# Optimization experiments

Measured on AMD Instinct MI355X. Metric: run time of the kernel, lower is better.

The kernel has to match this reference:

```python
import jax, jax.numpy as jnp
import numpy as np

B, T, C, H = 2, 2048, 1024, 16
D = C // H  # head_dim = 64


def wheel_softmax(scores):
    """Wheel-arithmetic softmax: total division, bot (0/0) positions -> 0.
    Rows that are entirely -inf yield sum==0 -> bot -> filled with 0.0,
    matching wheel_out.to_numpy_safe(bot_fill=0.0, inf_fill=0.0)."""
    m = jnp.max(scores, axis=-1, keepdims=True)
    safe_m = jnp.where(jnp.isfinite(m), m, 0.0)
    e = jnp.exp(scores - safe_m)          # -inf entries -> 0
    z = jnp.sum(e, axis=-1, keepdims=True)
    ok = z > 0
    return jnp.where(ok, e / jnp.where(ok, z, 1.0), 0.0)


def setup_inputs() -> dict:
    key = jax.random.key(0)
    ks = jax.random.split(key, 12)
    s = 1.0 / np.sqrt(C)
    inp = {
        "query": jax.random.normal(ks[0], (B, T, C), jnp.float32),
        "key": jax.random.normal(ks[1], (B, T, C), jnp.float32),
        "value": jax.random.normal(ks[2], (B, T, C), jnp.float32),
        "q_w": jax.random.normal(ks[3], (C, C), jnp.float32) * s,
        "q_b": jax.random.normal(ks[4], (C,), jnp.float32) * 0.01,
        "k_w": jax.random.normal(ks[5], (C, C), jnp.float32) * s,
        "k_b": jax.random.normal(ks[6], (C,), jnp.float32) * 0.01,
        "v_w": jax.random.normal(ks[7], (C, C), jnp.float32) * s,
        "v_b": jax.random.normal(ks[8], (C,), jnp.float32) * 0.01,
        "o_w": jax.random.normal(ks[9], (C, C), jnp.float32) * s,
        "o_b": jax.random.normal(ks[10], (C,), jnp.float32) * 0.01,
        "key_padding_mask": jax.random.randint(ks[11], (B, T), 0, 2).astype(bool),
    }
    return inp


def reference(query, key, value, q_w, q_b, k_w, k_b, v_w, v_b, o_w, o_b, key_padding_mask):
    scale = D ** -0.5
    def proj(x, w, b):
        # nn.Linear: x @ w.T + b ; reshape to [B,H,T,D]
        y = jnp.einsum("btc,oc->bto", x, w) + b
        return y.reshape(B, T, H, D).transpose(0, 2, 1, 3)
    Q = proj(query, q_w, q_b)
    K = proj(key, k_w, k_b)
    V = proj(value, v_w, v_b)
    scores = jnp.einsum("bhqd,bhkd->bhqk", Q, K) * scale
    scores = jnp.where(key_padding_mask[:, None, None, :], -jnp.inf, scores)
    weights = wheel_softmax(scores)  # dropout=0 -> identity
    out = jnp.einsum("bhqk,bhkd->bhqd", weights, V)
    out = out.transpose(0, 2, 1, 3).reshape(B, T, C)
    out = jnp.einsum("btc,oc->bto", out, o_w) + o_b
    return (out, weights)
```

## Files before the change

kernel.cpp:

```cpp
#include <hip/hip_runtime.h>
#include <math.h>


typedef _Float16 f16;
typedef _Float16 f16x2 __attribute__((ext_vector_type(2)));
typedef _Float16 f16x4 __attribute__((ext_vector_type(4)));
typedef _Float16 f16x8 __attribute__((ext_vector_type(8)));
typedef float  f32x2  __attribute__((ext_vector_type(2)));
typedef float  f32x4  __attribute__((ext_vector_type(4)));

#define MFMAH(a, b, c)  __builtin_amdgcn_mfma_f32_16x16x32_f16((a), (b), (c), 0, 0, 0)

__device__ __forceinline__ void gload16(void* lds, const void* g) {
  __builtin_amdgcn_global_load_lds((__attribute__((address_space(1))) void*)(g),
                                   (__attribute__((address_space(3))) void*)(lds),
                                   16, 0, 0);
}

__global__ __launch_bounds__(256) void conv_f16(const float* __restrict__ q, const float* __restrict__ k,
                                                const float* __restrict__ v, const float* __restrict__ qw,
                                                const float* __restrict__ kw, const float* __restrict__ vw,
                                                const float* __restrict__ ow, f16* __restrict__ xf) {
  long long i = ((long long)blockIdx.x * 256 + threadIdx.x) * 4;
  const float* src;
  long long off;
  if (i < 4194304)       { src = q;  off = 0; }
  else if (i < 8388608)  { src = k;  off = 4194304; }
  else if (i < 12582912) { src = v;  off = 8388608; }
  else if (i < 13631488) { src = qw; off = 12582912; }
  else if (i < 14680064) { src = kw; off = 13631488; }
  else if (i < 15728640) { src = vw; off = 14680064; }
  else                   { src = ow; off = 15728640; }
  f32x4 val = *(const f32x4*)(src + (i - off));
  f16x4 h;
#pragma unroll
  for (int r = 0; r < 4; ++r) h[r] = (f16)val[r];
  *(f16x4*)(xf + i) = h;
}

__device__ __forceinline__ void stage_tile(f16* lds, const f16* g, int row0, int kc, int tid) {
#pragma unroll
  for (int j = 0; j < 2; ++j) {
    int chunk = j * 256 + tid;
    int r = chunk >> 2, cpos = chunk & 3;
    int csrc = cpos ^ ((r >> 1) & 3);
    gload16((char*)lds + chunk * 16,
            (const char*)(g + (size_t)(row0 + r) * 1024 + kc) + csrc * 16);
  }
}

__device__ __forceinline__ f16x8 frag_ld(const f16* lds, int row, int g) {
  int pos = g ^ ((row >> 1) & 3);
  return *(const f16x8*)((const char*)lds + row * 64 + pos * 16);
}

__device__ __forceinline__ void gemm_core(const f16* A, const f16* X, int o0, int t0, int tid,
                                          f16* sA, f16* sB, f32x4 acc[4][4]) {
  int wid = tid >> 6, lane = tid & 63;
  int wm = wid >> 1, wn = wid & 1, g = lane >> 4, r15 = lane & 15;
  for (int kc = 0; kc < 1024; kc += 32) {
    __syncthreads();
    stage_tile(sA, A, o0, kc, tid);
    stage_tile(sB, X, t0, kc, tid);
    __syncthreads();
    f16x8 a[4], x[4];
#pragma unroll
    for (int f = 0; f < 4; ++f) {
      a[f] = frag_ld(sA, wm * 64 + f * 16 + r15, g);
      x[f] = frag_ld(sB, wn * 64 + f * 16 + r15, g);
    }
#pragma unroll
    for (int fm = 0; fm < 4; ++fm)
#pragma unroll
      for (int fn = 0; fn < 4; ++fn)
        acc[fm][fn] = MFMAH(a[fm], x[fn], acc[fm][fn]);
  }
}

__global__ __launch_bounds__(256) void gemm_qkv(const f16* __restrict__ xf,
                                                const float* __restrict__ q_b, const float* __restrict__ k_b,
                                                const float* __restrict__ v_b,
                                                f16* __restrict__ Qf, f16* __restrict__ Kf,
                                                f16* __restrict__ VT2) {
  __shared__ f16 sA[4096], sB[4096];
  int z = blockIdx.z;
  int tid = threadIdx.x;
  int wid = tid >> 6, lane = tid & 63;
  int wm = wid >> 1, wn = wid & 1, g = lane >> 4, r15 = lane & 15;
  f32x4 acc[4][4] = {};
  if (z == 2) {
    const f16* X = xf + 8388608;
    const f16* W = xf + 14680064;
    int o0 = blockIdx.x * 128, t0 = blockIdx.y * 128;
    gemm_core(X, W, t0, o0, tid, sA, sB, acc);
#pragma unroll
    for (int fm = 0; fm < 4; ++fm)
#pragma unroll
      for (int fn = 0; fn < 4; ++fn) {
        int tb = t0 + wm * 64 + fm * 16 + 4 * g;
        int o  = o0 + wn * 64 + fn * 16 + r15;
        int bb = tb >> 11, tl = tb & 2047, hh = o >> 6, dd = o & 63;
        int ch = tl >> 5, c = tl & 31;
        int slotbase = (c < 16) ? ((c >> 2) << 3) : ((((c - 16) >> 2) << 3) + 4);
        float bo = v_b[o];
        f16x4 v4;
#pragma unroll
        for (int r = 0; r < 4; ++r) v4[r] = (f16)(acc[fm][fn][r] + bo);
        *(f16x4*)(VT2 + ((((size_t)bb * 16 + hh) * 64 + ch) * 64 + dd) * 32 + slotbase) = v4;
      }
  } else {
    const f16* A = xf + (z ? 13631488 : 12582912);
    const f16* X = xf + (z ? 4194304 : 0);
    const float* bias = z ? k_b : q_b;
    f16* Yf = z ? Kf : Qf;
    float scale = z ? 1.0f : 0.125f;
    int o0 = blockIdx.x * 128, t0 = blockIdx.y * 128;
    gemm_core(A, X, o0, t0, tid, sA, sB, acc);
#pragma unroll
    for (int fm = 0; fm < 4; ++fm)
#pragma unroll
      for (int fn = 0; fn < 4; ++fn) {
        int ob = o0 + wm * 64 + fm * 16 + 4 * g;
        int t  = t0 + wn * 64 + fn * 16 + r15;
        int bb = t >> 11, tl = t & 2047, hh = ob >> 6, dd = ob & 63;
        size_t base = (((size_t)bb * 16 + hh) * 2048 + tl) * 64 + dd;
        f16x4 vh;
#pragma unroll
        for (int r = 0; r < 4; ++r)
          vh[r] = (f16)((acc[fm][fn][r] + bias[ob + r]) * scale);
        *(f16x4*)(Yf + base) = vh;
      }
  }
}

__global__ __launch_bounds__(256) void gemm_o(const f16* __restrict__ xf, const f16* __restrict__ Abuf,
                                              const float* __restrict__ o_b, float* __restrict__ OutF) {
  __shared__ f16 sA[4096], sB[4096];
  const f16* A = xf + 15728640;
  int tid = threadIdx.x;
  int o0 = blockIdx.x * 128, t0 = blockIdx.y * 128;
  int wid = tid >> 6, lane = tid & 63;
  int wm = wid >> 1, wn = wid & 1, g = lane >> 4, r15 = lane & 15;
  f32x4 acc[4][4] = {};
  gemm_core(A, Abuf, o0, t0, tid, sA, sB, acc);
#pragma unroll
  for (int fm = 0; fm < 4; ++fm)
#pragma unroll
    for (int fn = 0; fn < 4; ++fn) {
      int ob = o0 + wm * 64 + fm * 16 + 4 * g;
      int t  = t0 + wn * 64 + fn * 16 + r15;
      f32x4 v;
#pragma unroll
      for (int r = 0; r < 4; ++r) v[r] = acc[fm][fn][r] + o_b[ob + r];
      *(f32x4*)(OutF + (size_t)t * 1024 + ob) = v;
    }
}

__global__ __launch_bounds__(512, 4) void attn_kernel(
    const f16* __restrict__ Qf, const f16* __restrict__ Kf,
    const f16* __restrict__ VT2, const int* __restrict__ mask,
    float* __restrict__ wout, f16* __restrict__ Abuf) {
  __shared__ f16 kstage[8][2][1024];
  __shared__ f16 pvh[8][16][72];
  __shared__ float ps[128];
  __shared__ float rz[16];
  int tid = threadIdx.x;
  int wid = tid >> 6, lane = tid & 63;
  int g = lane >> 4, r15 = lane & 15;
  int qt = blockIdx.x & 127, bh = blockIdx.x >> 7;
  int b = bh >> 4, h = bh & 15;
  int q0 = qt * 16;

  if (blockIdx.x & 1) __builtin_amdgcn_s_sleep(24);

  const f16* qp = Qf + ((size_t)bh * 2048 + q0 + r15) * 64 + 8 * g;
  f16x8 qh0 = *(const f16x8*)(qp);
  f16x8 qh1 = *(const f16x8*)(qp + 32);

  const int* mp = mask + b * 2048 + wid * 256 + 4 * g;
  unsigned long long mb = 0;
#pragma unroll
  for (int t = 0; t < 16; ++t) {
    int4 ma = *(const int4*)(mp + t * 16);
    mb |= ((ma.x ? 1ull : 0ull) << (4 * t)) | ((ma.y ? 1ull : 0ull) << (4 * t + 1)) |
          ((ma.z ? 1ull : 0ull) << (4 * t + 2)) | ((ma.w ? 1ull : 0ull) << (4 * t + 3));
  }

  f16* kb0 = &kstage[wid][0][0];
  f16* kb1 = &kstage[wid][1][0];
  const f16* ksrcA = Kf + ((size_t)bh * 2048 + wid * 256 + (lane >> 3)) * 64 +
                     (((lane & 7) ^ ((lane >> 3) & 7)) * 8);
  const f16* ksrcB = ksrcA + 8 * 64;

  gload16(kb0, ksrcA);
  gload16(kb0 + 512, ksrcB);
  gload16(kb1, ksrcA + 1024);
  gload16(kb1 + 512, ksrcB + 1024);
  asm volatile("s_waitcnt vmcnt(2)" ::: "memory");
  int key = r15 & 7;
  f16x8 c0 = *(const f16x8*)(kb0 + r15 * 64 + ((g ^ key) * 8));
  f16x8 c1 = *(const f16x8*)(kb0 + r15 * 64 + (((g + 4) ^ key) * 8));

  float psum = 0.f;
  f16x4 p16[16];
#pragma unroll
  for (int s = 0; s < 16; ++s) {
    if (s < 14) {
      asm volatile("s_waitcnt lgkmcnt(0)" ::: "memory");
      f16* nb = (s & 1) ? kb1 : kb0;
      gload16(nb, ksrcA + (s + 2) * 1024);
      gload16(nb + 512, ksrcB + (s + 2) * 1024);
    }
    f16x8 n0, n1;
    if (s < 15) {
      if (s < 14) asm volatile("s_waitcnt vmcnt(2)" ::: "memory");
      else        asm volatile("s_waitcnt vmcnt(0)" ::: "memory");
      const f16* nt = ((s + 1) & 1) ? kb1 : kb0;
      n0 = *(const f16x8*)(nt + r15 * 64 + ((g ^ key) * 8));
      n1 = *(const f16x8*)(nt + r15 * 64 + (((g + 4) ^ key) * 8));
    }
    f32x4 sc = {0.f, 0.f, 0.f, 0.f};
    sc = MFMAH(c0, qh0, sc);
    sc = MFMAH(c1, qh1, sc);
    f16x4 pk;
#pragma unroll
    for (int r = 0; r < 4; ++r) {
      float e = ((mb >> (4 * s + r)) & 1) ? 0.f : __expf(sc[r]);
      psum += e;
      pk[r] = (f16)e;
    }
    p16[s] = pk;
    c0 = n0;
    c1 = n1;
  }

  psum += __shfl_xor(psum, 16);
  psum += __shfl_xor(psum, 32);
  if (lane < 16) ps[lane * 8 + wid] = psum;
  __syncthreads();

  if (tid < 128) {
    float z = ps[tid];
#pragma unroll
    for (int m = 1; m <= 4; m <<= 1) z += __shfl_xor(z, m);
    if ((tid & 7) == 0) rz[tid >> 3] = (z > 0.f) ? 1.0f / z : 0.0f;
  }
  __syncthreads();

  f32x4 acc[4] = {};
  {
    float rzv = rz[r15];
    float* wb = wout + ((size_t)bh * 2048 + q0 + r15) * 2048 + wid * 256 + 4 * g;
    const f16* vb = VT2 + (((size_t)bh * 64 + wid * 8) * 64 + r15) * 32 + g * 8;
    f16x8 v0 = *(const f16x8*)(vb);
    f16x8 v1 = *(const f16x8*)(vb + 512);
    f16x8 v2 = *(const f16x8*)(vb + 1024);
    f16x8 v3 = *(const f16x8*)(vb + 1536);
#pragma unroll
    for (int t = 0; t < 8; ++t) {
      f16x8 n0, n1, n2, n3;
      if (t < 7) {
        const f16* nvb = vb + (t + 1) * 2048;
        n0 = *(const f16x8*)(nvb);
        n1 = *(const f16x8*)(nvb + 512);
        n2 = *(const f16x8*)(nvb + 1024);
        n3 = *(const f16x8*)(nvb + 1536);
      }
#pragma unroll
      for (int u = 0; u < 2; ++u) {
        int s = 2 * t + u;
        f16x4 pk = p16[s];
        f32x4 wv;
#pragma unroll
        for (int r = 0; r < 4; ++r) wv[r] = (float)pk[r] * rzv;
        __builtin_nontemporal_store(wv, (f32x4*)(wb + s * 16));
      }
      f16x8 af = __builtin_shufflevector(p16[2 * t], p16[2 * t + 1], 0, 1, 2, 3, 4, 5, 6, 7);
      acc[0] = MFMAH(af, v0, acc[0]);
      acc[1] = MFMAH(af, v1, acc[1]);
      acc[2] = MFMAH(af, v2, acc[2]);
      acc[3] = MFMAH(af, v3, acc[3]);
      v0 = n0; v1 = n1; v2 = n2; v3 = n3;
    }
#pragma unroll
    for (int dt = 0; dt < 4; ++dt)
#pragma unroll
      for (int r = 0; r < 4; ++r)
        pvh[wid][4 * g + r][dt * 16 + r15] = (f16)acc[dt][r];
  }
  __syncthreads();

  {
    int q = tid >> 5, d = (tid & 31) * 2;
    float a0 = 0.f, a1 = 0.f;
#pragma unroll
    for (int w8 = 0; w8 < 8; ++w8) {
      f16x2 v = *(const f16x2*)&pvh[w8][q][d];
      a0 += (float)v[0];
      a1 += (float)v[1];
    }
    float rzq = rz[q];
    f16x2 o2 = {(f16)(a0 * rzq), (f16)(a1 * rzq)};
    *(f16x2*)(Abuf + ((size_t)b * 2048 + q0 + q) * 1024 + h * 64 + d) = o2;
  }
}

extern "C" void kernel_launch(void* const* d_in, const int* in_sizes, int n_in,
                              void* d_out, int out_size, void* d_ws, size_t ws_size,
                              hipStream_t stream) {
  const float* query = (const float*)d_in[0];
  const float* key_i = (const float*)d_in[1];
  const float* value = (const float*)d_in[2];
  const float* q_w = (const float*)d_in[3];
  const float* q_b = (const float*)d_in[4];
  const float* k_w = (const float*)d_in[5];
  const float* k_b = (const float*)d_in[6];
  const float* v_w = (const float*)d_in[7];
  const float* v_b = (const float*)d_in[8];
  const float* o_w = (const float*)d_in[9];
  const float* o_b = (const float*)d_in[10];
  const int* mask = (const int*)d_in[11];
  float* out = (float*)d_out;
  float* wout = out + 4194304;

  const size_t XFB = 16777216ull * 2;
  const size_t QB = 4194304ull * 2;
  if (ws_size < XFB + 2 * QB) return;
  f16* xf = (f16*)d_ws;
  f16* Qf = (f16*)((char*)d_ws + XFB);
  f16* Kf = (f16*)((char*)d_ws + XFB + QB);
  f16* VT2 = xf;
  f16* Abuf = xf + 4194304;
  VT2 = (f16*)((char*)d_ws + XFB + 2 * QB - 0);
  VT2  = (f16*)((char*)d_ws + XFB + 2 * QB);
  Abuf = (f16*)((char*)d_ws + XFB + 3 * QB);
  if (ws_size < XFB + 4 * QB) return;

  conv_f16<<<16384, 256, 0, stream>>>(query, key_i, value, q_w, k_w, v_w, o_w, xf);
  gemm_qkv<<<dim3(8, 32, 3), 256, 0, stream>>>(xf, q_b, k_b, v_b, Qf, Kf, VT2);
  attn_kernel<<<4096, 512, 0, stream>>>(Qf, Kf, VT2, mask, wout, Abuf);
  gemm_o<<<dim3(8, 32), 256, 0, stream>>>(xf, Abuf, o_b, out);
}
```

Measured before the change: 264.2 us.

## Stage attention weights through LDS for row-contiguous coalesced stores

The attention kernel now writes the fp16 probabilities into a per-wave LDS scratch area that reuses the K staging buffer. It reads them back transposed so each lane stores 16-byte chunks along a row, and each row of the 2048-wide fp32 weights output gets 512 contiguous bytes instead of scattered 16-byte pieces. This targets write coalescing on the dominant weights-output traffic. It also raises the launch-bounds occupancy hint from 4 to 6, removes the s_sleep stagger on odd blocks, and tidies the workspace pointer setup. The costs are extra LDS traffic, a waitcnt, and possible register pressure from the higher occupancy target.

```diff
diff --git a/kernel.cpp b/kernel.cpp
--- a/kernel.cpp
+++ b/kernel.cpp
@@ -156,11 +156,11 @@
     }
 }
 
-__global__ __launch_bounds__(512, 4) void attn_kernel(
+__global__ __launch_bounds__(512, 6) void attn_kernel(
     const f16* __restrict__ Qf, const f16* __restrict__ Kf,
     const f16* __restrict__ VT2, const int* __restrict__ mask,
     float* __restrict__ wout, f16* __restrict__ Abuf) {
-  __shared__ f16 kstage[8][2][1024];
+  __shared__ char smemA[8][4224];
   __shared__ f16 pvh[8][16][72];
   __shared__ float ps[128];
   __shared__ float rz[16];
@@ -171,8 +171,6 @@
   int b = bh >> 4, h = bh & 15;
   int q0 = qt * 16;
 
-  if (blockIdx.x & 1) __builtin_amdgcn_s_sleep(24);
-
   const f16* qp = Qf + ((size_t)bh * 2048 + q0 + r15) * 64 + 8 * g;
   f16x8 qh0 = *(const f16x8*)(qp);
   f16x8 qh1 = *(const f16x8*)(qp + 32);
@@ -186,8 +184,8 @@
           ((ma.z ? 1ull : 0ull) << (4 * t + 2)) | ((ma.w ? 1ull : 0ull) << (4 * t + 3));
   }
 
-  f16* kb0 = &kstage[wid][0][0];
-  f16* kb1 = &kstage[wid][1][0];
+  f16* kb0 = (f16*)&smemA[wid][0];
+  f16* kb1 = (f16*)&smemA[wid][2048];
   const f16* ksrcA = Kf + ((size_t)bh * 2048 + wid * 256 + (lane >> 3)) * 64 +
                      (((lane & 7) ^ ((lane >> 3) & 7)) * 8);
   const f16* ksrcB = ksrcA + 8 * 64;
@@ -249,8 +247,9 @@
 
   f32x4 acc[4] = {};
   {
-    float rzv = rz[r15];
-    float* wb = wout + ((size_t)bh * 2048 + q0 + r15) * 2048 + wid * 256 + 4 * g;
+    char* pst = &smemA[wid][0];
+    int c5 = lane & 31, hi5 = lane >> 5;
+    float* wrowbase = wout + ((size_t)bh * 2048 + q0) * 2048 + wid * 256;
     const f16* vb = VT2 + (((size_t)bh * 64 + wid * 8) * 64 + r15) * 32 + g * 8;
     f16x8 v0 = *(const f16x8*)(vb);
     f16x8 v1 = *(const f16x8*)(vb + 512);
@@ -266,14 +265,26 @@
         n2 = *(const f16x8*)(nvb + 1024);
         n3 = *(const f16x8*)(nvb + 1536);
       }
-#pragma unroll
-      for (int u = 0; u < 2; ++u) {
-        int s = 2 * t + u;
-        f16x4 pk = p16[s];
-        f32x4 wv;
-#pragma unroll
-        for (int r = 0; r < 4; ++r) wv[r] = (float)pk[r] * rzv;
-        __builtin_nontemporal_store(wv, (f32x4*)(wb + s * 16));
+      if (t == 0 || t == 4) {
+        int hb = (t >> 2) * 8;
+#pragma unroll
+        for (int s2 = 0; s2 < 8; ++s2)
+          *(f16x4*)(pst + r15 * 264 + s2 * 32 + g * 8) = p16[hb + s2];
+        asm volatile("s_waitcnt lgkmcnt(0)" ::: "memory");
+      }
+      {
+        int hh2 = t >> 2, rbase = (t & 3) * 4;
+#pragma unroll
+        for (int u = 0; u < 2; ++u) {
+          int row = rbase + 2 * u + hi5;
+          f16x4 pv4 = *(const f16x4*)(pst + row * 264 + c5 * 8);
+          float rzr = rz[row];
+          f32x4 wv;
+#pragma unroll
+          for (int r = 0; r < 4; ++r) wv[r] = (float)pv4[r] * rzr;
+          __builtin_nontemporal_store(wv,
+              (f32x4*)(wrowbase + (size_t)row * 2048 + hh2 * 128 + 4 * c5));
+        }
       }
       f16x8 af = __builtin_shufflevector(p16[2 * t], p16[2 * t + 1], 0, 1, 2, 3, 4, 5, 6, 7);
       acc[0] = MFMAH(af, v0, acc[0]);
@@ -325,16 +336,12 @@
 
   const size_t XFB = 16777216ull * 2;
   const size_t QB = 4194304ull * 2;
-  if (ws_size < XFB + 2 * QB) return;
-  f16* xf = (f16*)d_ws;
-  f16* Qf = (f16*)((char*)d_ws + XFB);
-  f16* Kf = (f16*)((char*)d_ws + XFB + QB);
-  f16* VT2 = xf;
-  f16* Abuf = xf + 4194304;
-  VT2 = (f16*)((char*)d_ws + XFB + 2 * QB - 0);
-  VT2  = (f16*)((char*)d_ws + XFB + 2 * QB);
-  Abuf = (f16*)((char*)d_ws + XFB + 3 * QB);
   if (ws_size < XFB + 4 * QB) return;
+  f16* xf   = (f16*)d_ws;
+  f16* Qf   = (f16*)((char*)d_ws + XFB);
+  f16* Kf   = (f16*)((char*)d_ws + XFB + QB);
+  f16* VT2  = (f16*)((char*)d_ws + XFB + 2 * QB);
+  f16* Abuf = (f16*)((char*)d_ws + XFB + 3 * QB);
 
   conv_f16<<<16384, 256, 0, stream>>>(query, key_i, value, q_w, k_w, v_w, o_w, xf);
   gemm_qkv<<<dim3(8, 32, 3), 256, 0, stream>>>(xf, q_b, k_b, v_b, Qf, Kf, VT2);
```

Result: faster. 258.9 us (-2.0%).

## Split attention into row-sum pass and main pass with larger query tiles

Applied to the files above, without the earlier changes.

Replaces the single attention kernel with two kernels. The first computes per-row softmax normalizers using 128-query tiles per block, so each loaded K tile is reused across eight query groups. The second recomputes scores for 32-query tiles, normalizes them on the fly, writes the weights and does P·V, which doubles K/V reuse per block and keeps fewer probabilities in registers. The cost is computing QK^T twice plus an extra launch and a small Zinv buffer, in exchange for more K reuse and less register pressure.

```diff
diff --git a/kernel.cpp b/kernel.cpp
--- a/kernel.cpp
+++ b/kernel.cpp
@@ -10,6 +10,7 @@
 typedef float  f32x4  __attribute__((ext_vector_type(4)));
 
 #define MFMAH(a, b, c)  __builtin_amdgcn_mfma_f32_16x16x32_f16((a), (b), (c), 0, 0, 0)
+#define SB0() __builtin_amdgcn_sched_barrier(0)
 
 __device__ __forceinline__ void gload16(void* lds, const void* g) {
   __builtin_amdgcn_global_load_lds((__attribute__((address_space(1))) void*)(g),
@@ -156,26 +157,17 @@
     }
 }
 
-__global__ __launch_bounds__(512, 4) void attn_kernel(
+__global__ __launch_bounds__(512, 4) void attn_rowsum(
     const f16* __restrict__ Qf, const f16* __restrict__ Kf,
-    const f16* __restrict__ VT2, const int* __restrict__ mask,
-    float* __restrict__ wout, f16* __restrict__ Abuf) {
+    const int* __restrict__ mask, float* __restrict__ Zinv) {
   __shared__ f16 kstage[8][2][1024];
-  __shared__ f16 pvh[8][16][72];
-  __shared__ float ps[128];
-  __shared__ float rz[16];
+  __shared__ float ps[128][8];
   int tid = threadIdx.x;
   int wid = tid >> 6, lane = tid & 63;
   int g = lane >> 4, r15 = lane & 15;
-  int qt = blockIdx.x & 127, bh = blockIdx.x >> 7;
-  int b = bh >> 4, h = bh & 15;
-  int q0 = qt * 16;
-
-  if (blockIdx.x & 1) __builtin_amdgcn_s_sleep(24);
-
-  const f16* qp = Qf + ((size_t)bh * 2048 + q0 + r15) * 64 + 8 * g;
-  f16x8 qh0 = *(const f16x8*)(qp);
-  f16x8 qh1 = *(const f16x8*)(qp + 32);
+  int qt = blockIdx.x, bh = blockIdx.y;
+  int b = bh >> 4;
+  int q0 = qt * 128;
 
   const int* mp = mask + b * 2048 + wid * 256 + 4 * g;
   unsigned long long mb = 0;
@@ -185,123 +177,197 @@
     mb |= ((ma.x ? 1ull : 0ull) << (4 * t)) | ((ma.y ? 1ull : 0ull) << (4 * t + 1)) |
           ((ma.z ? 1ull : 0ull) << (4 * t + 2)) | ((ma.w ? 1ull : 0ull) << (4 * t + 3));
   }
-
+  f16x8 qf[8][2];
+#pragma unroll
+  for (int qg = 0; qg < 8; ++qg) {
+    const f16* qp = Qf + ((size_t)bh * 2048 + q0 + qg * 16 + r15) * 64 + 8 * g;
+    qf[qg][0] = *(const f16x8*)(qp);
+    qf[qg][1] = *(const f16x8*)(qp + 32);
+  }
+  SB0();
   f16* kb0 = &kstage[wid][0][0];
   f16* kb1 = &kstage[wid][1][0];
   const f16* ksrcA = Kf + ((size_t)bh * 2048 + wid * 256 + (lane >> 3)) * 64 +
                      (((lane & 7) ^ ((lane >> 3) & 7)) * 8);
-  const f16* ksrcB = ksrcA + 8 * 64;
-
-  gload16(kb0, ksrcA);
-  gload16(kb0 + 512, ksrcB);
-  gload16(kb1, ksrcA + 1024);
-  gload16(kb1 + 512, ksrcB + 1024);
-  asm volatile("s_waitcnt vmcnt(2)" ::: "memory");
+  const f16* ksrcB = ksrcA + 512;
+  gload16(kb0, ksrcA); gload16(kb0 + 512, ksrcB);
+  SB0();
+  gload16(kb1, ksrcA + 1024); gload16(kb1 + 512, ksrcB + 1024);
+  SB0();
+
+  float psum[8] = {};
   int key = r15 & 7;
-  f16x8 c0 = *(const f16x8*)(kb0 + r15 * 64 + ((g ^ key) * 8));
-  f16x8 c1 = *(const f16x8*)(kb0 + r15 * 64 + (((g + 4) ^ key) * 8));
-
-  float psum = 0.f;
-  f16x4 p16[16];
 #pragma unroll
   for (int s = 0; s < 16; ++s) {
+    if (s < 15) asm volatile("s_waitcnt vmcnt(2)" ::: "memory");
+    else        asm volatile("s_waitcnt vmcnt(0)" ::: "memory");
+    const f16* kt = (s & 1) ? kb1 : kb0;
+    f16x8 c0 = *(const f16x8*)(kt + r15 * 64 + ((g ^ key) * 8));
+    f16x8 c1 = *(const f16x8*)(kt + r15 * 64 + (((g + 4) ^ key) * 8));
+    asm volatile("s_waitcnt lgkmcnt(0)" ::: "memory");
     if (s < 14) {
-      asm volatile("s_waitcnt lgkmcnt(0)" ::: "memory");
       f16* nb = (s & 1) ? kb1 : kb0;
       gload16(nb, ksrcA + (s + 2) * 1024);
       gload16(nb + 512, ksrcB + (s + 2) * 1024);
     }
-    f16x8 n0, n1;
-    if (s < 15) {
-      if (s < 14) asm volatile("s_waitcnt vmcnt(2)" ::: "memory");
-      else        asm volatile("s_waitcnt vmcnt(0)" ::: "memory");
-      const f16* nt = ((s + 1) & 1) ? kb1 : kb0;
-      n0 = *(const f16x8*)(nt + r15 * 64 + ((g ^ key) * 8));
-      n1 = *(const f16x8*)(nt + r15 * 64 + (((g + 4) ^ key) * 8));
-    }
-    f32x4 sc = {0.f, 0.f, 0.f, 0.f};
-    sc = MFMAH(c0, qh0, sc);
-    sc = MFMAH(c1, qh1, sc);
-    f16x4 pk;
+    SB0();
+#pragma unroll
+    for (int qg = 0; qg < 8; ++qg) {
+      f32x4 sc = {0.f, 0.f, 0.f, 0.f};
+      sc = MFMAH(c0, qf[qg][0], sc);
+      sc = MFMAH(c1, qf[qg][1], sc);
+#pragma unroll
+      for (int r = 0; r < 4; ++r) {
+        float e = ((mb >> (4 * s + r)) & 1) ? 0.f : __expf(sc[r]);
+        psum[qg] += e;
+      }
+    }
+  }
+#pragma unroll
+  for (int qg = 0; qg < 8; ++qg) {
+    float z = psum[qg];
+    z += __shfl_xor(z, 16);
+    z += __shfl_xor(z, 32);
+    if (lane < 16) ps[qg * 16 + lane][wid] = z;
+  }
+  __syncthreads();
+  if (tid < 128) {
+    float z = 0.f;
+#pragma unroll
+    for (int w8 = 0; w8 < 8; ++w8) z += ps[tid][w8];
+    Zinv[(size_t)bh * 2048 + q0 + tid] = (z > 0.f) ? 1.0f / z : 0.0f;
+  }
+}
+
+__global__ __launch_bounds__(512, 4) void attn_main(
+    const f16* __restrict__ Qf, const f16* __restrict__ Kf,
+    const f16* __restrict__ VT2, const int* __restrict__ mask,
+    const float* __restrict__ Zinv, float* __restrict__ wout, f16* __restrict__ Abuf) {
+  __shared__ f16 kstage[8][2][1024];
+  __shared__ f16 qlds[2048];
+  __shared__ f16 pvh[8][32][72];
+  int tid = threadIdx.x;
+  int wid = tid >> 6, lane = tid & 63;
+  int g = lane >> 4, r15 = lane & 15;
+  int qt = blockIdx.x, bh = blockIdx.y;
+  int b = bh >> 4, h = bh & 15;
+  int q0 = qt * 32;
+
+  const int* mp = mask + b * 2048 + wid * 256 + 4 * g;
+  unsigned long long mb = 0;
+#pragma unroll
+  for (int t = 0; t < 16; ++t) {
+    int4 ma = *(const int4*)(mp + t * 16);
+    mb |= ((ma.x ? 1ull : 0ull) << (4 * t)) | ((ma.y ? 1ull : 0ull) << (4 * t + 1)) |
+          ((ma.z ? 1ull : 0ull) << (4 * t + 2)) | ((ma.w ? 1ull : 0ull) << (4 * t + 3));
+  }
+  float rz0 = Zinv[(size_t)bh * 2048 + q0 + r15];
+  float rz1 = Zinv[(size_t)bh * 2048 + q0 + 16 + r15];
+  if (wid < 4) {
+    int row = wid * 8 + (lane >> 3);
+    const f16* qsrc = Qf + ((size_t)bh * 2048 + q0 + row) * 64 + (((lane & 7) ^ (row & 7)) * 8);
+    gload16(qlds + wid * 512, qsrc);
+  }
+  SB0();
+  f16* kb0 = &kstage[wid][0][0];
+  f16* kb1 = &kstage[wid][1][0];
+  const f16* ksrcA = Kf + ((size_t)bh * 2048 + wid * 256 + (lane >> 3)) * 64 +
+                     (((lane & 7) ^ ((lane >> 3) & 7)) * 8);
+  const f16* ksrcB = ksrcA + 512;
+  gload16(kb0, ksrcA); gload16(kb0 + 512, ksrcB);
+  SB0();
+  gload16(kb1, ksrcA + 1024); gload16(kb1 + 512, ksrcB + 1024);
+  SB0();
+  asm volatile("s_waitcnt vmcnt(4)" ::: "memory");
+  __builtin_amdgcn_s_barrier();
+
+  int key = r15 & 7;
+  float* wb0 = wout + ((size_t)bh * 2048 + q0 + r15) * 2048 + wid * 256 + 4 * g;
+  float* wb1 = wb0 + (size_t)16 * 2048;
+  const f16* vb = VT2 + (((size_t)bh * 64 + wid * 8) * 64 + r15) * 32 + g * 8;
+
+  f32x4 acc0[4] = {}, acc1[4] = {};
+  f16x4 pp0, pp1;
+  f16x8 v0, v1, v2, v3;
+#pragma unroll
+  for (int s = 0; s < 16; ++s) {
+    if (s == 0)       asm volatile("s_waitcnt vmcnt(2)" ::: "memory");
+    else if (s == 1)  asm volatile("s_waitcnt vmcnt(8)" ::: "memory");
+    else if (s == 15) asm volatile("s_waitcnt vmcnt(8)" ::: "memory");
+    else              asm volatile("s_waitcnt vmcnt(10)" ::: "memory");
+    const f16* kt = (s & 1) ? kb1 : kb0;
+    f16x8 c0  = *(const f16x8*)(kt + r15 * 64 + ((g ^ key) * 8));
+    f16x8 c1  = *(const f16x8*)(kt + r15 * 64 + (((g + 4) ^ key) * 8));
+    f16x8 q00 = *(const f16x8*)(qlds + r15 * 64 + ((g ^ key) * 8));
+    f16x8 q01 = *(const f16x8*)(qlds + r15 * 64 + (((g + 4) ^ key) * 8));
+    f16x8 q10 = *(const f16x8*)(qlds + (16 + r15) * 64 + ((g ^ key) * 8));
+    f16x8 q11 = *(const f16x8*)(qlds + (16 + r15) * 64 + (((g + 4) ^ key) * 8));
+    asm volatile("s_waitcnt lgkmcnt(0)" ::: "memory");
+    if (s < 14) {
+      f16* nb = (s & 1) ? kb1 : kb0;
+      gload16(nb, ksrcA + (s + 2) * 1024);
+      gload16(nb + 512, ksrcB + (s + 2) * 1024);
+    }
+    SB0();
+    if ((s & 1) == 0) {
+      const f16* vp = vb + (s >> 1) * 2048;
+      v0 = *(const f16x8*)(vp);
+      v1 = *(const f16x8*)(vp + 512);
+      v2 = *(const f16x8*)(vp + 1024);
+      v3 = *(const f16x8*)(vp + 1536);
+    }
+    f32x4 s0 = {0.f, 0.f, 0.f, 0.f}, s1 = {0.f, 0.f, 0.f, 0.f};
+    s0 = MFMAH(c0, q00, s0);
+    s0 = MFMAH(c1, q01, s0);
+    s1 = MFMAH(c0, q10, s1);
+    s1 = MFMAH(c1, q11, s1);
+    f32x4 w0v, w1v;
+    f16x4 pk0, pk1;
 #pragma unroll
     for (int r = 0; r < 4; ++r) {
-      float e = ((mb >> (4 * s + r)) & 1) ? 0.f : __expf(sc[r]);
-      psum += e;
-      pk[r] = (f16)e;
-    }
-    p16[s] = pk;
-    c0 = n0;
-    c1 = n1;
-  }
-
-  psum += __shfl_xor(psum, 16);
-  psum += __shfl_xor(psum, 32);
-  if (lane < 16) ps[lane * 8 + wid] = psum;
+      float e0 = ((mb >> (4 * s + r)) & 1) ? 0.f : __expf(s0[r]);
+      float e1 = ((mb >> (4 * s + r)) & 1) ? 0.f : __expf(s1[r]);
+      float x0 = e0 * rz0, x1 = e1 * rz1;
+      w0v[r] = x0; pk0[r] = (f16)x0;
+      w1v[r] = x1; pk1[r] = (f16)x1;
+    }
+    __builtin_nontemporal_store(w0v, (f32x4*)(wb0 + s * 16));
+    __builtin_nontemporal_store(w1v, (f32x4*)(wb1 + s * 16));
+    if (s & 1) {
+      f16x8 af0 = __builtin_shufflevector(pp0, pk0, 0, 1, 2, 3, 4, 5, 6, 7);
+      f16x8 af1 = __builtin_shufflevector(pp1, pk1, 0, 1, 2, 3, 4, 5, 6, 7);
+      acc0[0] = MFMAH(af0, v0, acc0[0]);
+      acc1[0] = MFMAH(af1, v0, acc1[0]);
+      acc0[1] = MFMAH(af0, v1, acc0[1]);
+      acc1[1] = MFMAH(af1, v1, acc1[1]);
+      acc0[2] = MFMAH(af0, v2, acc0[2]);
+      acc1[2] = MFMAH(af1, v2, acc1[2]);
+      acc0[3] = MFMAH(af0, v3, acc0[3]);
+      acc1[3] = MFMAH(af1, v3, acc1[3]);
+    }
+    pp0 = pk0;
+    pp1 = pk1;
+  }
+
+#pragma unroll
+  for (int dt = 0; dt < 4; ++dt)
+#pragma unroll
+    for (int r = 0; r < 4; ++r) {
+      pvh[wid][4 * g + r][dt * 16 + r15] = (f16)acc0[dt][r];
+      pvh[wid][16 + 4 * g + r][dt * 16 + r15] = (f16)acc1[dt][r];
+    }
   __syncthreads();
 
-  if (tid < 128) {
-    float z = ps[tid];
-#pragma unroll
-    for (int m = 1; m <= 4; m <<= 1) z += __shfl_xor(z, m);
-    if ((tid & 7) == 0) rz[tid >> 3] = (z > 0.f) ? 1.0f / z : 0.0f;
-  }
-  __syncthreads();
-
-  f32x4 acc[4] = {};
   {
-    float rzv = rz[r15];
-    float* wb = wout + ((size_t)bh * 2048 + q0 + r15) * 2048 + wid * 256 + 4 * g;
-    const f16* vb = VT2 + (((size_t)bh * 64 + wid * 8) * 64 + r15) * 32 + g * 8;
-    f16x8 v0 = *(const f16x8*)(vb);
-    f16x8 v1 = *(const f16x8*)(vb + 512);
-    f16x8 v2 = *(const f16x8*)(vb + 1024);
-    f16x8 v3 = *(const f16x8*)(vb + 1536);
-#pragma unroll
-    for (int t = 0; t < 8; ++t) {
-      f16x8 n0, n1, n2, n3;
-      if (t < 7) {
-        const f16* nvb = vb + (t + 1) * 2048;
-        n0 = *(const f16x8*)(nvb);
-        n1 = *(const f16x8*)(nvb + 512);
-        n2 = *(const f16x8*)(nvb + 1024);
-        n3 = *(const f16x8*)(nvb + 1536);
-      }
-#pragma unroll
-      for (int u = 0; u < 2; ++u) {
-        int s = 2 * t + u;
-        f16x4 pk = p16[s];
-        f32x4 wv;
-#pragma unroll
-        for (int r = 0; r < 4; ++r) wv[r] = (float)pk[r] * rzv;
-        __builtin_nontemporal_store(wv, (f32x4*)(wb + s * 16));
-      }
-      f16x8 af = __builtin_shufflevector(p16[2 * t], p16[2 * t + 1], 0, 1, 2, 3, 4, 5, 6, 7);
-      acc[0] = MFMAH(af, v0, acc[0]);
-      acc[1] = MFMAH(af, v1, acc[1]);
-      acc[2] = MFMAH(af, v2, acc[2]);
-      acc[3] = MFMAH(af, v3, acc[3]);
-      v0 = n0; v1 = n1; v2 = n2; v3 = n3;
-    }
-#pragma unroll
-    for (int dt = 0; dt < 4; ++dt)
-#pragma unroll
-      for (int r = 0; r < 4; ++r)
-        pvh[wid][4 * g + r][dt * 16 + r15] = (f16)acc[dt][r];
-  }
-  __syncthreads();
-
-  {
-    int q = tid >> 5, d = (tid & 31) * 2;
-    float a0 = 0.f, a1 = 0.f;
+    int q = tid >> 4, d4 = (tid & 15) * 4;
+    float a0 = 0.f, a1 = 0.f, a2 = 0.f, a3 = 0.f;
 #pragma unroll
     for (int w8 = 0; w8 < 8; ++w8) {
-      f16x2 v = *(const f16x2*)&pvh[w8][q][d];
-      a0 += (float)v[0];
-      a1 += (float)v[1];
-    }
-    float rzq = rz[q];
-    f16x2 o2 = {(f16)(a0 * rzq), (f16)(a1 * rzq)};
-    *(f16x2*)(Abuf + ((size_t)b * 2048 + q0 + q) * 1024 + h * 64 + d) = o2;
+      f16x4 v = *(const f16x4*)&pvh[w8][q][d4];
+      a0 += (float)v[0]; a1 += (float)v[1]; a2 += (float)v[2]; a3 += (float)v[3];
+    }
+    f16x4 o4 = {(f16)a0, (f16)a1, (f16)a2, (f16)a3};
+    *(f16x4*)(Abuf + ((size_t)b * 2048 + q0 + q) * 1024 + h * 64 + d4) = o4;
   }
 }
 
@@ -325,19 +391,18 @@
 
   const size_t XFB = 16777216ull * 2;
   const size_t QB = 4194304ull * 2;
-  if (ws_size < XFB + 2 * QB) return;
-  f16* xf = (f16*)d_ws;
-  f16* Qf = (f16*)((char*)d_ws + XFB);
-  f16* Kf = (f16*)((char*)d_ws + XFB + QB);
-  f16* VT2 = xf;
-  f16* Abuf = xf + 4194304;
-  VT2 = (f16*)((char*)d_ws + XFB + 2 * QB - 0);
-  VT2  = (f16*)((char*)d_ws + XFB + 2 * QB);
-  Abuf = (f16*)((char*)d_ws + XFB + 3 * QB);
-  if (ws_size < XFB + 4 * QB) return;
+  const size_t ZB = 65536ull * 4;
+  if (ws_size < XFB + 4 * QB + ZB) return;
+  f16* xf    = (f16*)d_ws;
+  f16* Qf    = (f16*)((char*)d_ws + XFB);
+  f16* Kf    = (f16*)((char*)d_ws + XFB + QB);
+  f16* VT2   = (f16*)((char*)d_ws + XFB + 2 * QB);
+  f16* Abuf  = (f16*)((char*)d_ws + XFB + 3 * QB);
+  float* Zinv = (float*)((char*)d_ws + XFB + 4 * QB);
 
   conv_f16<<<16384, 256, 0, stream>>>(query, key_i, value, q_w, k_w, v_w, o_w, xf);
   gemm_qkv<<<dim3(8, 32, 3), 256, 0, stream>>>(xf, q_b, k_b, v_b, Qf, Kf, VT2);
-  attn_kernel<<<4096, 512, 0, stream>>>(Qf, Kf, VT2, mask, wout, Abuf);
+  attn_rowsum<<<dim3(16, 32), 512, 0, stream>>>(Qf, Kf, mask, Zinv);
+  attn_main<<<dim3(64, 32), 512, 0, stream>>>(Qf, Kf, VT2, mask, Zinv, wout, Abuf);
   gemm_o<<<dim3(8, 32), 256, 0, stream>>>(xf, Abuf, o_b, out);
 }
```

New measurement: 528.3 us. 2x slower.

## Split attention into row-sum pre-pass and streaming weight-writing main kernel

Applied to the files above, without the earlier changes.

Adds a separate kernel that computes softmax denominators (inverse row sums) for 128 queries per block, reusing each staged K tile across 8 query groups. The main attention kernel then reads the precomputed inverse sums, so it can normalize and stream the fp32 weights out inside the QK loop. This removes the two block-wide syncs and the deferred store phase, which lets the weight writes overlap with compute, and the occupancy hint is raised. The cost is computing QK^T and exp a second time plus an extra launch.

```diff
diff --git a/kernel.cpp b/kernel.cpp
--- a/kernel.cpp
+++ b/kernel.cpp
@@ -156,14 +156,90 @@
     }
 }
 
-__global__ __launch_bounds__(512, 4) void attn_kernel(
+__global__ __launch_bounds__(512, 4) void attn_rowsum(
+    const f16* __restrict__ Qf, const f16* __restrict__ Kf,
+    const int* __restrict__ mask, float* __restrict__ Zinv) {
+  __shared__ f16 kstage[8][2][1024];
+  __shared__ float ps[128][8];
+  int tid = threadIdx.x;
+  int wid = tid >> 6, lane = tid & 63;
+  int g = lane >> 4, r15 = lane & 15;
+  int qt = blockIdx.x, bh = blockIdx.y;
+  int b = bh >> 4;
+  int q0 = qt * 128;
+
+  const int* mp = mask + b * 2048 + wid * 256 + 4 * g;
+  unsigned long long mb = 0;
+#pragma unroll
+  for (int t = 0; t < 16; ++t) {
+    int4 ma = *(const int4*)(mp + t * 16);
+    mb |= ((ma.x ? 1ull : 0ull) << (4 * t)) | ((ma.y ? 1ull : 0ull) << (4 * t + 1)) |
+          ((ma.z ? 1ull : 0ull) << (4 * t + 2)) | ((ma.w ? 1ull : 0ull) << (4 * t + 3));
+  }
+  f16x8 qf[8][2];
+#pragma unroll
+  for (int qg = 0; qg < 8; ++qg) {
+    const f16* qp = Qf + ((size_t)bh * 2048 + q0 + qg * 16 + r15) * 64 + 8 * g;
+    qf[qg][0] = *(const f16x8*)(qp);
+    qf[qg][1] = *(const f16x8*)(qp + 32);
+  }
+  f16* kb0 = &kstage[wid][0][0];
+  f16* kb1 = &kstage[wid][1][0];
+  const f16* ksrcA = Kf + ((size_t)bh * 2048 + wid * 256 + (lane >> 3)) * 64 +
+                     (((lane & 7) ^ ((lane >> 3) & 7)) * 8);
+  const f16* ksrcB = ksrcA + 512;
+  gload16(kb0, ksrcA); gload16(kb0 + 512, ksrcB);
+  gload16(kb1, ksrcA + 1024); gload16(kb1 + 512, ksrcB + 1024);
+
+  float psum[8] = {};
+  int key = r15 & 7;
+#pragma unroll
+  for (int s = 0; s < 16; ++s) {
+    if (s < 15) asm volatile("s_waitcnt vmcnt(2)" ::: "memory");
+    else        asm volatile("s_waitcnt vmcnt(0)" ::: "memory");
+    const f16* kt = (s & 1) ? kb1 : kb0;
+    f16x8 c0 = *(const f16x8*)(kt + r15 * 64 + ((g ^ key) * 8));
+    f16x8 c1 = *(const f16x8*)(kt + r15 * 64 + (((g + 4) ^ key) * 8));
+    asm volatile("s_waitcnt lgkmcnt(0)" ::: "memory");
+    if (s < 14) {
+      f16* nb = (s & 1) ? kb1 : kb0;
+      gload16(nb, ksrcA + (s + 2) * 1024);
+      gload16(nb + 512, ksrcB + (s + 2) * 1024);
+    }
+#pragma unroll
+    for (int qg = 0; qg < 8; ++qg) {
+      f32x4 sc = {0.f, 0.f, 0.f, 0.f};
+      sc = MFMAH(c0, qf[qg][0], sc);
+      sc = MFMAH(c1, qf[qg][1], sc);
+#pragma unroll
+      for (int r = 0; r < 4; ++r) {
+        float e = ((mb >> (4 * s + r)) & 1) ? 0.f : __expf(sc[r]);
+        psum[qg] += e;
+      }
+    }
+  }
+#pragma unroll
+  for (int qg = 0; qg < 8; ++qg) {
+    float z = psum[qg];
+    z += __shfl_xor(z, 16);
+    z += __shfl_xor(z, 32);
+    if (lane < 16) ps[qg * 16 + lane][wid] = z;
+  }
+  __syncthreads();
+  if (tid < 128) {
+    float z = 0.f;
+#pragma unroll
+    for (int w8 = 0; w8 < 8; ++w8) z += ps[tid][w8];
+    Zinv[(size_t)bh * 2048 + q0 + tid] = (z > 0.f) ? 1.0f / z : 0.0f;
+  }
+}
+
+__global__ __launch_bounds__(512, 6) void attn_main(
     const f16* __restrict__ Qf, const f16* __restrict__ Kf,
     const f16* __restrict__ VT2, const int* __restrict__ mask,
-    float* __restrict__ wout, f16* __restrict__ Abuf) {
+    const float* __restrict__ Zinv, float* __restrict__ wout, f16* __restrict__ Abuf) {
   __shared__ f16 kstage[8][2][1024];
   __shared__ f16 pvh[8][16][72];
-  __shared__ float ps[128];
-  __shared__ float rz[16];
   int tid = threadIdx.x;
   int wid = tid >> 6, lane = tid & 63;
   int g = lane >> 4, r15 = lane & 15;
@@ -171,11 +247,11 @@
   int b = bh >> 4, h = bh & 15;
   int q0 = qt * 16;
 
-  if (blockIdx.x & 1) __builtin_amdgcn_s_sleep(24);
-
   const f16* qp = Qf + ((size_t)bh * 2048 + q0 + r15) * 64 + 8 * g;
   f16x8 qh0 = *(const f16x8*)(qp);
   f16x8 qh1 = *(const f16x8*)(qp + 32);
+
+  float rzv = Zinv[(size_t)bh * 2048 + q0 + r15];
 
   const int* mp = mask + b * 2048 + wid * 256 + 4 * g;
   unsigned long long mb = 0;
@@ -190,7 +266,7 @@
   f16* kb1 = &kstage[wid][1][0];
   const f16* ksrcA = Kf + ((size_t)bh * 2048 + wid * 256 + (lane >> 3)) * 64 +
                      (((lane & 7) ^ ((lane >> 3) & 7)) * 8);
-  const f16* ksrcB = ksrcA + 8 * 64;
+  const f16* ksrcB = ksrcA + 512;
 
   gload16(kb0, ksrcA);
   gload16(kb0 + 512, ksrcB);
@@ -201,7 +277,7 @@
   f16x8 c0 = *(const f16x8*)(kb0 + r15 * 64 + ((g ^ key) * 8));
   f16x8 c1 = *(const f16x8*)(kb0 + r15 * 64 + (((g + 4) ^ key) * 8));
 
-  float psum = 0.f;
+  float* wb = wout + ((size_t)bh * 2048 + q0 + r15) * 2048 + wid * 256 + 4 * g;
   f16x4 p16[16];
 #pragma unroll
   for (int s = 0; s < 16; ++s) {
@@ -213,8 +289,9 @@
     }
     f16x8 n0, n1;
     if (s < 15) {
-      if (s < 14) asm volatile("s_waitcnt vmcnt(2)" ::: "memory");
-      else        asm volatile("s_waitcnt vmcnt(0)" ::: "memory");
+      if (s == 0)      asm volatile("s_waitcnt vmcnt(2)" ::: "memory");
+      else if (s < 14) asm volatile("s_waitcnt vmcnt(3)" ::: "memory");
+      else             asm volatile("s_waitcnt vmcnt(1)" ::: "memory");
       const f16* nt = ((s + 1) & 1) ? kb1 : kb0;
       n0 = *(const f16x8*)(nt + r15 * 64 + ((g ^ key) * 8));
       n1 = *(const f16x8*)(nt + r15 * 64 + (((g + 4) ^ key) * 8));
@@ -222,35 +299,23 @@
     f32x4 sc = {0.f, 0.f, 0.f, 0.f};
     sc = MFMAH(c0, qh0, sc);
     sc = MFMAH(c1, qh1, sc);
+    f32x4 wv;
     f16x4 pk;
 #pragma unroll
     for (int r = 0; r < 4; ++r) {
       float e = ((mb >> (4 * s + r)) & 1) ? 0.f : __expf(sc[r]);
-      psum += e;
-      pk[r] = (f16)e;
+      float x = e * rzv;
+      wv[r] = x;
+      pk[r] = (f16)x;
     }
     p16[s] = pk;
+    __builtin_nontemporal_store(wv, (f32x4*)(wb + s * 16));
     c0 = n0;
     c1 = n1;
   }
 
-  psum += __shfl_xor(psum, 16);
-  psum += __shfl_xor(psum, 32);
-  if (lane < 16) ps[lane * 8 + wid] = psum;
-  __syncthreads();
-
-  if (tid < 128) {
-    float z = ps[tid];
-#pragma unroll
-    for (int m = 1; m <= 4; m <<= 1) z += __shfl_xor(z, m);
-    if ((tid & 7) == 0) rz[tid >> 3] = (z > 0.f) ? 1.0f / z : 0.0f;
-  }
-  __syncthreads();
-
   f32x4 acc[4] = {};
   {
-    float rzv = rz[r15];
-    float* wb = wout + ((size_t)bh * 2048 + q0 + r15) * 2048 + wid * 256 + 4 * g;
     const f16* vb = VT2 + (((size_t)bh * 64 + wid * 8) * 64 + r15) * 32 + g * 8;
     f16x8 v0 = *(const f16x8*)(vb);
     f16x8 v1 = *(const f16x8*)(vb + 512);
@@ -266,15 +331,6 @@
         n2 = *(const f16x8*)(nvb + 1024);
         n3 = *(const f16x8*)(nvb + 1536);
       }
-#pragma unroll
-      for (int u = 0; u < 2; ++u) {
-        int s = 2 * t + u;
-        f16x4 pk = p16[s];
-        f32x4 wv;
-#pragma unroll
-        for (int r = 0; r < 4; ++r) wv[r] = (float)pk[r] * rzv;
-        __builtin_nontemporal_store(wv, (f32x4*)(wb + s * 16));
-      }
       f16x8 af = __builtin_shufflevector(p16[2 * t], p16[2 * t + 1], 0, 1, 2, 3, 4, 5, 6, 7);
       acc[0] = MFMAH(af, v0, acc[0]);
       acc[1] = MFMAH(af, v1, acc[1]);
@@ -299,8 +355,7 @@
       a0 += (float)v[0];
       a1 += (float)v[1];
     }
-    float rzq = rz[q];
-    f16x2 o2 = {(f16)(a0 * rzq), (f16)(a1 * rzq)};
+    f16x2 o2 = {(f16)a0, (f16)a1};
     *(f16x2*)(Abuf + ((size_t)b * 2048 + q0 + q) * 1024 + h * 64 + d) = o2;
   }
 }
@@ -325,19 +380,18 @@
 
   const size_t XFB = 16777216ull * 2;
   const size_t QB = 4194304ull * 2;
-  if (ws_size < XFB + 2 * QB) return;
-  f16* xf = (f16*)d_ws;
-  f16* Qf = (f16*)((char*)d_ws + XFB);
-  f16* Kf = (f16*)((char*)d_ws + XFB + QB);
-  f16* VT2 = xf;
-  f16* Abuf = xf + 4194304;
-  VT2 = (f16*)((char*)d_ws + XFB + 2 * QB - 0);
-  VT2  = (f16*)((char*)d_ws + XFB + 2 * QB);
-  Abuf = (f16*)((char*)d_ws + XFB + 3 * QB);
-  if (ws_size < XFB + 4 * QB) return;
+  const size_t ZB = 65536ull * 4;
+  if (ws_size < XFB + 4 * QB + ZB) return;
+  f16* xf    = (f16*)d_ws;
+  f16* Qf    = (f16*)((char*)d_ws + XFB);
+  f16* Kf    = (f16*)((char*)d_ws + XFB + QB);
+  f16* VT2   = (f16*)((char*)d_ws + XFB + 2 * QB);
+  f16* Abuf  = (f16*)((char*)d_ws + XFB + 3 * QB);
+  float* Zinv = (float*)((char*)d_ws + XFB + 4 * QB);
 
   conv_f16<<<16384, 256, 0, stream>>>(query, key_i, value, q_w, k_w, v_w, o_w, xf);
   gemm_qkv<<<dim3(8, 32, 3), 256, 0, stream>>>(xf, q_b, k_b, v_b, Qf, Kf, VT2);
-  attn_kernel<<<4096, 512, 0, stream>>>(Qf, Kf, VT2, mask, wout, Abuf);
+  attn_rowsum<<<dim3(16, 32), 512, 0, stream>>>(Qf, Kf, mask, Zinv);
+  attn_main<<<4096, 512, 0, stream>>>(Qf, Kf, VT2, mask, Zinv, wout, Abuf);
   gemm_o<<<dim3(8, 32), 256, 0, stream>>>(xf, Abuf, o_b, out);
 }
```

Result: slower. 668.0 us (+152.8%).
